# Performance work log

Hardware: AMD Instinct MI355X
Metric: run time of the kernel (lower is better)

The kernel has to match this reference:

```python
import jax, jax.numpy as jnp
import numpy as np
import math

NUM_BUCKETS = 32
MAX_DISTANCE = 128
N_HEADS = 16
D_KV = 64
ATTN_SCALE = True


def _relative_position_bucket(relative_position, num_buckets=NUM_BUCKETS, max_distance=MAX_DISTANCE):
    # bidirectional (encoder) variant
    nb = num_buckets // 2
    buckets = (relative_position > 0).astype(jnp.int32) * nb
    rp = jnp.abs(relative_position)
    max_exact = nb // 2
    is_small = rp < max_exact
    rp_large = max_exact + (
        jnp.log(rp.astype(jnp.float32) / max_exact)
        / math.log(max_distance / max_exact)
        * (nb - max_exact)
    ).astype(jnp.int32)
    rp_large = jnp.minimum(rp_large, nb - 1)
    buckets = buckets + jnp.where(is_small, rp, rp_large)
    return buckets


def compute_bias(rel_bias_emb, q_len, k_len):
    ctx = jnp.arange(q_len)[:, None]
    mem = jnp.arange(k_len)[None, :]
    bucket = _relative_position_bucket(mem - ctx)  # [q,k] int32 in [0,32)
    values = rel_bias_emb[bucket]                  # [q,k,H]
    return jnp.transpose(values, (2, 0, 1))[None]  # [1,H,q,k]


def setup_inputs() -> dict:
    key = jax.random.key(0)
    k1, k2, k3, k4 = jax.random.split(key, 4)
    B, S, D = 2, 2048, 1024
    return {
        "hidden_states": jax.random.normal(k1, (B, S, D), jnp.float32),
        "attention_mask": jnp.ones((B, 1, S, S), jnp.float32),
        "W_qkv": jax.random.normal(k2, (D, 3 * D), jnp.float32) * 0.02,
        "W_o": jax.random.normal(k3, (D, D), jnp.float32) * 0.02,
        "rel_bias_emb": jax.random.normal(k4, (NUM_BUCKETS, N_HEADS), jnp.float32) * 0.02,
    }


def reference(hidden_states, attention_mask, W_qkv, W_o, rel_bias_emb):
    B, S, D = hidden_states.shape
    # fused QKV projection (no bias), then split as in split_tensor_along_last_dim
    qkv = jnp.einsum("bsd,de->bse", hidden_states, W_qkv)
    q, k, v = jnp.split(qkv, 3, axis=-1)
    # [b,s,H*d] -> [b,H,s,d]
    def to_heads(t):
        return jnp.transpose(t.reshape(B, S, N_HEADS, D_KV), (0, 2, 1, 3))
    q, k, v = to_heads(q), to_heads(k), to_heads(v)
    scores = jnp.einsum("bhqd,bhkd->bhqk", q, k)
    if ATTN_SCALE:
        scores = scores / math.sqrt(D_KV)
    position_bias = compute_bias(rel_bias_emb, S, S)  # [1,H,S,S]
    scores = scores * attention_mask + (-10000.0 * (1.0 - attention_mask) + position_bias)
    probs = jax.nn.softmax(scores, axis=-1)  # dropout = eval mode (identity)
    ctx = jnp.einsum("bhqk,bhkd->bhqd", probs, v)
    ctx = jnp.transpose(ctx, (0, 2, 1, 3)).reshape(B, S, N_HEADS * D_KV)
    attn_output = jnp.einsum("bse,ed->bsd", ctx, W_o)
    return attn_output
```

## Files before the change

kernel.cpp:

```cpp
#include <hip/hip_runtime.h>
#include <cstdint>

#define DEV static __device__ __forceinline__

typedef __bf16 bf16x8 __attribute__((ext_vector_type(8)));
typedef __bf16 bf16x4 __attribute__((ext_vector_type(4)));
typedef short  s16x4  __attribute__((ext_vector_type(4)));
typedef float  f32x4  __attribute__((ext_vector_type(4)));

DEV unsigned short f32_bf16(float f) {
  union { float f; unsigned u; } v; v.f = f;
  unsigned r = v.u + 0x7FFFu + ((v.u >> 16) & 1u);
  return (unsigned short)(r >> 16);
}

DEV void gload16(const void* g, void* lds) {
  __builtin_amdgcn_global_load_lds((__attribute__((address_space(1))) void*)g,
                                   (__attribute__((address_space(3))) void*)lds,
                                   16, 0, 0);
}

DEV float bcast_lane(float v, int srclane) {
  union { float f; int i; } u; u.f = v;
  u.i = __builtin_amdgcn_ds_bpermute(srclane << 2, u.i);
  return u.f;
}

DEV f32x4 mfma16_bf16(bf16x4 a, bf16x4 b, f32x4 c) {
  union { bf16x4 h; s16x4 s; } ua, ub; ua.h = a; ub.h = b;
#if __has_builtin(__builtin_amdgcn_mfma_f32_16x16x16bf16_1k)
  return __builtin_amdgcn_mfma_f32_16x16x16bf16_1k(ua.s, ub.s, c, 0, 0, 0);
#else
  f32x4 d;
  asm("v_mfma_f32_16x16x16_bf16 %0, %1, %2, %3" : "=v"(d) : "v"(ua.s), "v"(ub.s), "v"(c));
  return d;
#endif
}

__global__ void cast_and_check(const float* __restrict__ x, unsigned short* __restrict__ y,
                               const float* __restrict__ m, int* __restrict__ flag) {
  int bx = blockIdx.x;
  if (bx < 4096) {
    int i = bx * 256 + threadIdx.x;
    float4 v = ((const float4*)x)[i];
    uint2 o;
    o.x = (unsigned)f32_bf16(v.x) | ((unsigned)f32_bf16(v.y) << 16);
    o.y = (unsigned)f32_bf16(v.z) | ((unsigned)f32_bf16(v.w) << 16);
    ((uint2*)y)[i] = o;
  } else {
    size_t i = ((size_t)(bx - 4096) * 256 + threadIdx.x) * 4;
    float4 v = *(const float4*)(m + i);
    if (v.x != 1.0f || v.y != 1.0f || v.z != 1.0f || v.w != 1.0f) atomicOr(flag, 1);
  }
}

__global__ void transpose_cast2(const float* __restrict__ W1, unsigned short* __restrict__ WT1,
                                const float* __restrict__ W2, unsigned short* __restrict__ WT2) {
  __shared__ float t[64][65];
  int bx = blockIdx.x;
  const float* W; unsigned short* WT; int N, kb, nb;
  if (bx < 768) { W = W1; WT = WT1; N = 3072; kb = bx & 15; nb = bx >> 4; }
  else { bx -= 768; W = W2; WT = WT2; N = 1024; kb = bx & 15; nb = bx >> 4; }
  const int K = 1024;
  int k0 = kb * 64, n0 = nb * 64;
  int tn = threadIdx.x & 63, tk = threadIdx.x >> 6;
#pragma unroll
  for (int i = 0; i < 64; i += 4)
    t[tk + i][tn] = W[(size_t)(k0 + tk + i) * N + n0 + tn];
  __syncthreads();
  int k2 = (threadIdx.x & 31) * 2, n = threadIdx.x >> 5;
#pragma unroll
  for (int i = 0; i < 64; i += 8) {
    int nn = n + i;
    unsigned o = (unsigned)f32_bf16(t[k2][nn]) | ((unsigned)f32_bf16(t[k2 + 1][nn]) << 16);
    *(unsigned*)&WT[(size_t)(n0 + nn) * K + k0 + k2] = o;
  }
}

template <int MODE, int TN>
__global__ void __launch_bounds__(256) gemm_bt(const unsigned short* __restrict__ A,
                                               const unsigned short* __restrict__ BT,
                                               float* __restrict__ Cout,
                                               unsigned short* __restrict__ Qb,
                                               unsigned short* __restrict__ Kb,
                                               unsigned short* __restrict__ VTb,
                                               int M, int N, int K) {
  constexpr int NT = TN / 32;
  __shared__ __align__(16) unsigned short As[128 * 32];
  __shared__ __align__(16) unsigned short Bs[TN * 32];
  const int tid = threadIdx.x, wave = tid >> 6, lane = tid & 63;
  const int l = lane & 15, quad = lane >> 4;
  const int wm = (wave & 1) * 64, wn = (wave >> 1) * (TN >> 1);
  const int bm = blockIdx.x, bn = blockIdx.y;

  const int srowA = wave * 32 + (lane >> 2);
  const int sswzA = ((lane & 3) ^ (srowA & 3)) * 8;
  const int srowB = (TN == 128) ? srowA : (wave * 16 + (lane >> 2));
  const int sswzB = ((lane & 3) ^ (srowB & 3)) * 8;
  const unsigned short* pA = A + (size_t)(bm * 128 + srowA) * K + sswzA;
  const unsigned short* pB = BT + (size_t)(bn * TN + srowB) * K + sswzB;
  unsigned short* ldsA0 = &As[(wave * 32) * 32];
  unsigned short* ldsA1 = &As[(wave * 32 + 16) * 32];
  unsigned short* ldsB0 = &Bs[((TN == 128 ? wave * 32 : wave * 16)) * 32];
  unsigned short* ldsB1 = &Bs[(wave * 32 + 16) * 32];

  f32x4 acc[4][NT];
#pragma unroll
  for (int i = 0; i < 4; i++)
#pragma unroll
    for (int j = 0; j < NT; j++) { f32x4 z = {0.f, 0.f, 0.f, 0.f}; acc[i][j] = z; }

  for (int kt = 0; kt < K; kt += 32) {
    __syncthreads();
    gload16(pA, ldsA0);
    gload16(pA + (size_t)16 * K, ldsA1);
    gload16(pB, ldsB0);
    if (TN == 128) gload16(pB + (size_t)16 * K, ldsB1);
    pA += 32; pB += 32;
    __syncthreads();
    bf16x8 af[4], bv[NT];
#pragma unroll
    for (int mt = 0; mt < 4; mt++) {
      int r = wm + mt * 16 + l;
      af[mt] = *(const bf16x8*)&As[r * 32 + ((quad ^ (r & 3)) * 8)];
    }
#pragma unroll
    for (int nt = 0; nt < NT; nt++) {
      int r = wn + nt * 16 + l;
      bv[nt] = *(const bf16x8*)&Bs[r * 32 + ((quad ^ (r & 3)) * 8)];
    }
#pragma unroll
    for (int mt = 0; mt < 4; mt++)
#pragma unroll
      for (int nt = 0; nt < NT; nt++)
        acc[mt][nt] = __builtin_amdgcn_mfma_f32_16x16x32_bf16(af[mt], bv[nt], acc[mt][nt], 0, 0, 0);
  }

#pragma unroll
  for (int nt = 0; nt < NT; nt++) {
    const int col = bn * TN + wn + nt * 16 + l;
#pragma unroll
    for (int mt = 0; mt < 4; mt++) {
      const int row0 = bm * 128 + wm + mt * 16 + quad * 4;
      if (MODE == 0) {
#pragma unroll
        for (int r = 0; r < 4; r++)
          Cout[(size_t)(row0 + r) * N + col] = acc[mt][nt][r];
      } else {
        const int bb = row0 >> 11, s = row0 & 2047;
        if (col < 2048) {
          unsigned short* dst = (col < 1024) ? Qb : Kb;
          const int c = col & 1023;
          const size_t off = ((size_t)(bb * 16 + (c >> 6)) * 2048 + s) * 64 + (c & 63);
#pragma unroll
          for (int r = 0; r < 4; r++)
            dst[off + (size_t)r * 64] = f32_bf16(acc[mt][nt][r]);
        } else {
          const int c = col - 2048;
          const size_t off = ((size_t)(bb * 16 + (c >> 6)) * 64 + (c & 63)) * 2048 + s;
          bf16x4 pk;
#pragma unroll
          for (int r = 0; r < 4; r++) pk[r] = (__bf16)acc[mt][nt][r];
          *(bf16x4*)&VTb[off] = pk;
        }
      }
    }
  }
}

__global__ void __launch_bounds__(512, 2) attn(const unsigned short* __restrict__ Qb,
                                               const unsigned short* __restrict__ Kb,
                                               const unsigned short* __restrict__ VTb,
                                               const float* __restrict__ mask,
                                               const float* __restrict__ emb,
                                               const int* __restrict__ mflag,
                                               unsigned short* __restrict__ ctx) {
  __shared__ __align__(16) unsigned short KV[2][16384];
  __shared__ float biasLUT[512];
  __shared__ float Lbuf[128];

  const float LOG2E = 1.4426950408889634f;
  const float c1 = 0.125f * LOG2E;
  const float C2 = 10000.0f * LOG2E;
  const int tid = threadIdx.x, wave = tid >> 6, lane = tid & 63;
  const int g = wave >> 2, gw = wave & 3;
  const int l = lane & 15, quad = lane >> 4;
  const int qt = blockIdx.x & 15, bh = blockIdx.x >> 4;
  const int b = bh >> 4, h = bh & 15;
  const int q0 = qt * 128;

  {
    int rel = tid - 256;
    int rp = rel < 0 ? -rel : rel;
    int off = rp < 8 ? rp
                     : 8 + (rp >= 12) + (rp >= 16) + (rp >= 23) + (rp >= 32) +
                           (rp >= 46) + (rp >= 64) + (rp >= 91);
    int bucket = (rel > 0 ? 16 : 0) + off;
    biasLUT[tid] = emb[bucket * 16 + h] * LOG2E;
  }
  const float satL = emb[15 * 16 + h] * LOG2E;
  const float satH = emb[31 * 16 + h] * LOG2E;
  const int masked = *mflag;

  const unsigned short* qbg = Qb  + ((size_t)(b * 16 + h) * 2048 + q0) * 64;
  const unsigned short* kbg = Kb  + (size_t)(b * 16 + h) * 2048 * 64;
  const unsigned short* vtb = VTb + (size_t)(b * 16 + h) * 64 * 2048;
  const float* mbase = mask + (size_t)b * 2048 * 2048;

  const int rw8 = lane >> 3, c8 = lane & 7;
  const int rw16 = lane >> 4, c16 = lane & 15;

  if (wave < 4) {
#pragma unroll
    for (int j = 0; j < 4; j++) {
      int row = wave * 32 + j * 8 + rw8;
      gload16(qbg + (size_t)row * 64 + ((c8 ^ (row & 7)) * 8), &KV[0][(wave * 32 + j * 8) * 64]);
    }
  }
  __syncthreads();
  bf16x8 qf[2][2];
#pragma unroll
  for (int mtq = 0; mtq < 2; mtq++)
#pragma unroll
    for (int ks = 0; ks < 2; ks++) {
      int row = gw * 32 + mtq * 16 + l;
      qf[mtq][ks] = *(const bf16x8*)&KV[0][row * 64 + (((ks * 4 + quad) ^ (row & 7)) * 8)];
    }

  float lr[2] = {0.f, 0.f};
  f32x4 Oa[2][4];
#pragma unroll
  for (int mt = 0; mt < 2; mt++)
#pragma unroll
    for (int dt = 0; dt < 4; dt++) { f32x4 z = {0.f, 0.f, 0.f, 0.f}; Oa[mt][dt] = z; }

  unsigned short* Ks  = &KV[g][0];
  unsigned short* VTs = &KV[g][8192];

  for (int t = 0; t < 8; t++) {
    const int k0 = (g * 8 + t) * 128;
    __syncthreads();
#pragma unroll
    for (int j = 0; j < 4; j++) {
      int row = gw * 32 + j * 8 + rw8;
      gload16(kbg + (size_t)(k0 + row) * 64 + ((c8 ^ (row & 7)) * 8),
              &Ks[(gw * 32 + j * 8) * 64]);
    }
#pragma unroll
    for (int j = 0; j < 4; j++) {
      int drow = gw * 16 + j * 4 + rw16;
      gload16(vtb + (size_t)drow * 2048 + k0 + ((c16 ^ (drow & 7)) * 8),
              &VTs[(gw * 16 + j * 4) * 128]);
    }
    __syncthreads();

    const int d0 = k0 - q0;
    const bool sat = (d0 >= 256) || (d0 <= -256);
    const float bias_u = d0 > 0 ? satH : satL;
    const int ibase = 256 + d0 + quad * 4 - gw * 32 - l;
    bf16x4 pa[2][8];

#pragma unroll
    for (int ntk = 0; ntk < 8; ntk++) {
      int row = ntk * 16 + l;
      bf16x8 kf0 = *(const bf16x8*)&Ks[row * 64 + ((quad ^ (row & 7)) * 8)];
      bf16x8 kf1 = *(const bf16x8*)&Ks[row * 64 + (((4 + quad) ^ (row & 7)) * 8)];
#pragma unroll
      for (int mtq = 0; mtq < 2; mtq++) {
        f32x4 s = {0.f, 0.f, 0.f, 0.f};
        s = __builtin_amdgcn_mfma_f32_16x16x32_bf16(kf0, qf[mtq][0], s, 0, 0, 0);
        s = __builtin_amdgcn_mfma_f32_16x16x32_bf16(kf1, qf[mtq][1], s, 0, 0, 0);

        const int ib = ibase - mtq * 16 + ntk * 16;
        if (!masked) {
          if (sat) {
#pragma unroll
            for (int r = 0; r < 4; r++) s[r] = fmaf(s[r], c1, bias_u);
          } else {
#pragma unroll
            for (int r = 0; r < 4; r++) s[r] = fmaf(s[r], c1, biasLUT[ib + r]);
          }
        } else {
          const int qg = q0 + gw * 32 + mtq * 16 + l;
          const int kg = k0 + ntk * 16 + quad * 4;
          float4 mv4 = *(const float4*)&mbase[(size_t)qg * 2048 + kg];
#pragma unroll
          for (int r = 0; r < 4; r++) {
            float mv = r == 0 ? mv4.x : (r == 1 ? mv4.y : (r == 2 ? mv4.z : mv4.w));
            float bias = sat ? bias_u : biasLUT[ib + r];
            s[r] = fmaf(s[r], mv * c1, fmaf(mv, C2, bias - C2));
          }
        }
        bf16x4 pk;
        float ls = 0.f;
#pragma unroll
        for (int r = 0; r < 4; r++) {
          float p = __builtin_amdgcn_exp2f(s[r]);
          ls += p;
          pk[r] = (__bf16)p;
        }
        lr[mtq] += ls;
        pa[mtq][ntk] = pk;
      }
    }

#pragma unroll
    for (int ntk = 0; ntk < 8; ntk++) {
      bf16x4 vf[4];
#pragma unroll
      for (int dt = 0; dt < 4; dt++) {
        int drow = dt * 16 + l;
        int ch = (ntk * 2 + (quad >> 1)) ^ (l & 7);
        vf[dt] = *(const bf16x4*)&VTs[drow * 128 + ch * 8 + (quad & 1) * 4];
      }
#pragma unroll
      for (int mtq = 0; mtq < 2; mtq++)
#pragma unroll
        for (int dt = 0; dt < 4; dt++)
          Oa[mtq][dt] = mfma16_bf16(pa[mtq][ntk], vf[dt], Oa[mtq][dt]);
    }
  }

#pragma unroll
  for (int mtq = 0; mtq < 2; mtq++) {
    float v = lr[mtq];
    v += __shfl_xor(v, 16);
    v += __shfl_xor(v, 32);
    lr[mtq] = v;
  }

  float* Obuf = (float*)&KV[1][0];
  __syncthreads();
  if (g == 1) {
#pragma unroll
    for (int mt = 0; mt < 2; mt++) {
#pragma unroll
      for (int dt = 0; dt < 4; dt++) {
        const int qc = gw * 8 + mt * 4 + quad;
        *(f32x4*)&Obuf[(dt * 16 + l) * 128 + ((qc ^ (l & 7)) * 4)] = Oa[mt][dt];
      }
      if (quad == 0) Lbuf[gw * 32 + mt * 16 + l] = lr[mt];
    }
  }
  __syncthreads();
  if (g == 0) {
    float inv[2];
#pragma unroll
    for (int mt = 0; mt < 2; mt++)
      inv[mt] = 1.0f / (lr[mt] + Lbuf[gw * 32 + mt * 16 + l]);
#pragma unroll
    for (int mt = 0; mt < 2; mt++)
#pragma unroll
      for (int dt = 0; dt < 4; dt++) {
        const int qc = gw * 8 + mt * 4 + quad;
        f32x4 o = Oa[mt][dt];
        o += *(const f32x4*)&Obuf[(dt * 16 + l) * 128 + ((qc ^ (l & 7)) * 4)];
#pragma unroll
        for (int r = 0; r < 4; r++) {
          float i_bc = bcast_lane(inv[mt], quad * 4 + r);
          const int qg = q0 + gw * 32 + mt * 16 + quad * 4 + r;
          ctx[(size_t)(b * 2048 + qg) * 1024 + h * 64 + dt * 16 + l] =
              f32_bf16(o[r] * i_bc);
        }
      }
  }
}

extern "C" void kernel_launch(void* const* d_in, const int* in_sizes, int n_in,
                              void* d_out, int out_size, void* d_ws, size_t ws_size,
                              hipStream_t stream) {
  const float* hs   = (const float*)d_in[0];
  const float* mask = (const float*)d_in[1];
  const float* wqkv = (const float*)d_in[2];
  const float* wo   = (const float*)d_in[3];
  const float* emb  = (const float*)d_in[4];
  float* out = (float*)d_out;

  char* ws = (char*)d_ws;
  unsigned short* hB  = (unsigned short*)(ws);
  unsigned short* ctx = (unsigned short*)(ws);
  unsigned short* wqT = (unsigned short*)(ws + 8388608);
  unsigned short* woT = (unsigned short*)(ws + 14680064);
  unsigned short* Qb  = (unsigned short*)(ws + 16777216);
  unsigned short* Kb  = (unsigned short*)(ws + 25165824);
  unsigned short* VTb = (unsigned short*)(ws + 33554432);
  int* mflag          = (int*)(ws + 41943040);
  if (ws_size < 41943044) return;

  hipMemsetAsync(mflag, 0, 4, stream);
  cast_and_check<<<12288, 256, 0, stream>>>(hs, hB, mask, mflag);
  transpose_cast2<<<1024, 256, 0, stream>>>(wqkv, wqT, wo, woT);
  gemm_bt<2, 128><<<dim3(32, 24), 256, 0, stream>>>(hB, wqT, nullptr, Qb, Kb, VTb, 4096, 3072, 1024);
  attn<<<512, 512, 0, stream>>>(Qb, Kb, VTb, mask, emb, mflag, ctx);
  gemm_bt<0, 64><<<dim3(32, 16), 256, 0, stream>>>(ctx, woT, out, nullptr, nullptr, nullptr, 4096, 1024, 1024);
}
```

Measured before the change: 234.8 us.

## Restructure attention into 4-wave blocks with 64x64 tiles and prescaled Q

```diff
diff --git a/kernel.cpp b/kernel.cpp
--- a/kernel.cpp
+++ b/kernel.cpp
@@ -7,6 +7,8 @@
 typedef __bf16 bf16x4 __attribute__((ext_vector_type(4)));
 typedef short  s16x4  __attribute__((ext_vector_type(4)));
 typedef float  f32x4  __attribute__((ext_vector_type(4)));
+
+#define C1L 0.18033688f
 
 DEV unsigned short f32_bf16(float f) {
   union { float f; unsigned u; } v; v.f = f;
@@ -150,11 +152,12 @@
         const int bb = row0 >> 11, s = row0 & 2047;
         if (col < 2048) {
           unsigned short* dst = (col < 1024) ? Qb : Kb;
+          const float sc = (col < 1024) ? C1L : 1.0f;
           const int c = col & 1023;
           const size_t off = ((size_t)(bb * 16 + (c >> 6)) * 2048 + s) * 64 + (c & 63);
 #pragma unroll
           for (int r = 0; r < 4; r++)
-            dst[off + (size_t)r * 64] = f32_bf16(acc[mt][nt][r]);
+            dst[off + (size_t)r * 64] = f32_bf16(acc[mt][nt][r] * sc);
         } else {
           const int c = col - 2048;
           const size_t off = ((size_t)(bb * 16 + (c >> 6)) * 64 + (c & 63)) * 2048 + s;
@@ -168,35 +171,36 @@
   }
 }
 
-__global__ void __launch_bounds__(512, 2) attn(const unsigned short* __restrict__ Qb,
+__global__ void __launch_bounds__(256, 2) attn(const unsigned short* __restrict__ Qb,
                                                const unsigned short* __restrict__ Kb,
                                                const unsigned short* __restrict__ VTb,
                                                const float* __restrict__ mask,
                                                const float* __restrict__ emb,
                                                const int* __restrict__ mflag,
                                                unsigned short* __restrict__ ctx) {
-  __shared__ __align__(16) unsigned short KV[2][16384];
+  __shared__ __align__(16) unsigned short KVbuf[16384];
   __shared__ float biasLUT[512];
   __shared__ float Lbuf[128];
+  unsigned short* Ks  = KVbuf;
+  unsigned short* VTs = KVbuf + 8192;
 
   const float LOG2E = 1.4426950408889634f;
-  const float c1 = 0.125f * LOG2E;
   const float C2 = 10000.0f * LOG2E;
   const int tid = threadIdx.x, wave = tid >> 6, lane = tid & 63;
-  const int g = wave >> 2, gw = wave & 3;
+  const int qi = wave >> 1, kj = wave & 1;
   const int l = lane & 15, quad = lane >> 4;
   const int qt = blockIdx.x & 15, bh = blockIdx.x >> 4;
   const int b = bh >> 4, h = bh & 15;
   const int q0 = qt * 128;
 
-  {
-    int rel = tid - 256;
+  for (int i = tid; i < 512; i += 256) {
+    int rel = i - 256;
     int rp = rel < 0 ? -rel : rel;
     int off = rp < 8 ? rp
                      : 8 + (rp >= 12) + (rp >= 16) + (rp >= 23) + (rp >= 32) +
                            (rp >= 46) + (rp >= 64) + (rp >= 91);
     int bucket = (rel > 0 ? 16 : 0) + off;
-    biasLUT[tid] = emb[bucket * 16 + h] * LOG2E;
+    biasLUT[i] = emb[bucket * 16 + h] * LOG2E;
   }
   const float satL = emb[15 * 16 + h] * LOG2E;
   const float satH = emb[31 * 16 + h] * LOG2E;
@@ -210,85 +214,78 @@
   const int rw8 = lane >> 3, c8 = lane & 7;
   const int rw16 = lane >> 4, c16 = lane & 15;
 
-  if (wave < 4) {
+#pragma unroll
+  for (int j = 0; j < 4; j++) {
+    int row = wave * 32 + j * 8 + rw8;
+    gload16(qbg + (size_t)row * 64 + ((c8 ^ (row & 7)) * 8), &Ks[(wave * 32 + j * 8) * 64]);
+  }
+  __syncthreads();
+  bf16x8 qf[4][2];
+#pragma unroll
+  for (int mtq = 0; mtq < 4; mtq++)
+#pragma unroll
+    for (int ks = 0; ks < 2; ks++) {
+      int row = qi * 64 + mtq * 16 + l;
+      qf[mtq][ks] = *(const bf16x8*)&Ks[row * 64 + (((ks * 4 + quad) ^ (row & 7)) * 8)];
+    }
+
+  float lr[4] = {0.f, 0.f, 0.f, 0.f};
+  f32x4 Oa[4][4];
+#pragma unroll
+  for (int mt = 0; mt < 4; mt++)
+#pragma unroll
+    for (int dt = 0; dt < 4; dt++) { f32x4 z = {0.f, 0.f, 0.f, 0.f}; Oa[mt][dt] = z; }
+
+  for (int t = 0; t < 16; t++) {
+    const int k0 = t * 128;
+    __syncthreads();
 #pragma unroll
     for (int j = 0; j < 4; j++) {
       int row = wave * 32 + j * 8 + rw8;
-      gload16(qbg + (size_t)row * 64 + ((c8 ^ (row & 7)) * 8), &KV[0][(wave * 32 + j * 8) * 64]);
-    }
-  }
-  __syncthreads();
-  bf16x8 qf[2][2];
-#pragma unroll
-  for (int mtq = 0; mtq < 2; mtq++)
-#pragma unroll
-    for (int ks = 0; ks < 2; ks++) {
-      int row = gw * 32 + mtq * 16 + l;
-      qf[mtq][ks] = *(const bf16x8*)&KV[0][row * 64 + (((ks * 4 + quad) ^ (row & 7)) * 8)];
-    }
-
-  float lr[2] = {0.f, 0.f};
-  f32x4 Oa[2][4];
-#pragma unroll
-  for (int mt = 0; mt < 2; mt++)
-#pragma unroll
-    for (int dt = 0; dt < 4; dt++) { f32x4 z = {0.f, 0.f, 0.f, 0.f}; Oa[mt][dt] = z; }
-
-  unsigned short* Ks  = &KV[g][0];
-  unsigned short* VTs = &KV[g][8192];
-
-  for (int t = 0; t < 8; t++) {
-    const int k0 = (g * 8 + t) * 128;
+      gload16(kbg + (size_t)(k0 + row) * 64 + ((c8 ^ (row & 7)) * 8),
+              &Ks[(wave * 32 + j * 8) * 64]);
+    }
+#pragma unroll
+    for (int j = 0; j < 4; j++) {
+      int drow = wave * 16 + j * 4 + rw16;
+      gload16(vtb + (size_t)drow * 2048 + k0 + ((c16 ^ (drow & 7)) * 8),
+              &VTs[(wave * 16 + j * 4) * 128]);
+    }
     __syncthreads();
-#pragma unroll
-    for (int j = 0; j < 4; j++) {
-      int row = gw * 32 + j * 8 + rw8;
-      gload16(kbg + (size_t)(k0 + row) * 64 + ((c8 ^ (row & 7)) * 8),
-              &Ks[(gw * 32 + j * 8) * 64]);
-    }
-#pragma unroll
-    for (int j = 0; j < 4; j++) {
-      int drow = gw * 16 + j * 4 + rw16;
-      gload16(vtb + (size_t)drow * 2048 + k0 + ((c16 ^ (drow & 7)) * 8),
-              &VTs[(gw * 16 + j * 4) * 128]);
-    }
-    __syncthreads();
-
-    const int d0 = k0 - q0;
-    const bool sat = (d0 >= 256) || (d0 <= -256);
-    const float bias_u = d0 > 0 ? satH : satL;
-    const int ibase = 256 + d0 + quad * 4 - gw * 32 - l;
-    bf16x4 pa[2][8];
-
-#pragma unroll
-    for (int ntk = 0; ntk < 8; ntk++) {
-      int row = ntk * 16 + l;
+
+    bf16x4 pa[4][4];
+#pragma unroll
+    for (int ntk = 0; ntk < 4; ntk++) {
+      const int row = kj * 64 + ntk * 16 + l;
       bf16x8 kf0 = *(const bf16x8*)&Ks[row * 64 + ((quad ^ (row & 7)) * 8)];
       bf16x8 kf1 = *(const bf16x8*)&Ks[row * 64 + (((4 + quad) ^ (row & 7)) * 8)];
 #pragma unroll
-      for (int mtq = 0; mtq < 2; mtq++) {
-        f32x4 s = {0.f, 0.f, 0.f, 0.f};
+      for (int mtq = 0; mtq < 4; mtq++) {
+        const int base16 = (k0 + kj * 64 + ntk * 16) - (q0 + qi * 64 + mtq * 16);
+        const bool sat = (base16 >= 106) || (base16 <= -106);
+        const float bias_u = base16 > 0 ? satH : satL;
+        const int ib = 256 + base16 + quad * 4 - l;
+        f32x4 s;
+        if (masked) {
+          f32x4 z = {0.f, 0.f, 0.f, 0.f}; s = z;
+        } else if (sat) {
+          s[0] = bias_u; s[1] = bias_u; s[2] = bias_u; s[3] = bias_u;
+        } else {
+#pragma unroll
+          for (int r = 0; r < 4; r++) s[r] = biasLUT[ib + r];
+        }
         s = __builtin_amdgcn_mfma_f32_16x16x32_bf16(kf0, qf[mtq][0], s, 0, 0, 0);
         s = __builtin_amdgcn_mfma_f32_16x16x32_bf16(kf1, qf[mtq][1], s, 0, 0, 0);
 
-        const int ib = ibase - mtq * 16 + ntk * 16;
-        if (!masked) {
-          if (sat) {
-#pragma unroll
-            for (int r = 0; r < 4; r++) s[r] = fmaf(s[r], c1, bias_u);
-          } else {
-#pragma unroll
-            for (int r = 0; r < 4; r++) s[r] = fmaf(s[r], c1, biasLUT[ib + r]);
-          }
-        } else {
-          const int qg = q0 + gw * 32 + mtq * 16 + l;
-          const int kg = k0 + ntk * 16 + quad * 4;
+        if (masked) {
+          const int qg = q0 + qi * 64 + mtq * 16 + l;
+          const int kg = k0 + kj * 64 + ntk * 16 + quad * 4;
           float4 mv4 = *(const float4*)&mbase[(size_t)qg * 2048 + kg];
 #pragma unroll
           for (int r = 0; r < 4; r++) {
             float mv = r == 0 ? mv4.x : (r == 1 ? mv4.y : (r == 2 ? mv4.z : mv4.w));
             float bias = sat ? bias_u : biasLUT[ib + r];
-            s[r] = fmaf(s[r], mv * c1, fmaf(mv, C2, bias - C2));
+            s[r] = fmaf(s[r], mv, fmaf(mv, C2, bias - C2));
           }
         }
         bf16x4 pk;
@@ -305,16 +302,16 @@
     }
 
 #pragma unroll
-    for (int ntk = 0; ntk < 8; ntk++) {
+    for (int ntk = 0; ntk < 4; ntk++) {
       bf16x4 vf[4];
 #pragma unroll
       for (int dt = 0; dt < 4; dt++) {
         int drow = dt * 16 + l;
-        int ch = (ntk * 2 + (quad >> 1)) ^ (l & 7);
-        vf[dt] = *(const bf16x4*)&VTs[drow * 128 + ch * 8 + (quad & 1) * 4];
+        int ck = kj * 8 + ntk * 2 + (quad >> 1);
+        vf[dt] = *(const bf16x4*)&VTs[drow * 128 + ((ck ^ (l & 7)) * 8) + (quad & 1) * 4];
       }
 #pragma unroll
-      for (int mtq = 0; mtq < 2; mtq++)
+      for (int mtq = 0; mtq < 4; mtq++)
 #pragma unroll
         for (int dt = 0; dt < 4; dt++)
           Oa[mtq][dt] = mfma16_bf16(pa[mtq][ntk], vf[dt], Oa[mtq][dt]);
@@ -322,45 +319,45 @@
   }
 
 #pragma unroll
-  for (int mtq = 0; mtq < 2; mtq++) {
+  for (int mtq = 0; mtq < 4; mtq++) {
     float v = lr[mtq];
     v += __shfl_xor(v, 16);
     v += __shfl_xor(v, 32);
     lr[mtq] = v;
   }
 
-  float* Obuf = (float*)&KV[1][0];
+  float* Obuf = (float*)KVbuf;
   __syncthreads();
-  if (g == 1) {
-#pragma unroll
-    for (int mt = 0; mt < 2; mt++) {
+  if (kj == 1) {
+#pragma unroll
+    for (int mtq = 0; mtq < 4; mtq++) {
+#pragma unroll
+      for (int dt = 0; dt < 4; dt++)
+#pragma unroll
+        for (int r = 0; r < 4; r++) {
+          const int q = qi * 64 + mtq * 16 + quad * 4 + r;
+          Obuf[q * 64 + dt * 16 + l] = Oa[mtq][dt][r];
+        }
+      if (quad == 0) Lbuf[qi * 64 + mtq * 16 + l] = lr[mtq];
+    }
+  }
+  __syncthreads();
+  if (kj == 0) {
+    float inv[4];
+#pragma unroll
+    for (int mtq = 0; mtq < 4; mtq++)
+      inv[mtq] = 1.0f / (lr[mtq] + Lbuf[qi * 64 + mtq * 16 + l]);
+#pragma unroll
+    for (int mtq = 0; mtq < 4; mtq++)
 #pragma unroll
       for (int dt = 0; dt < 4; dt++) {
-        const int qc = gw * 8 + mt * 4 + quad;
-        *(f32x4*)&Obuf[(dt * 16 + l) * 128 + ((qc ^ (l & 7)) * 4)] = Oa[mt][dt];
-      }
-      if (quad == 0) Lbuf[gw * 32 + mt * 16 + l] = lr[mt];
-    }
-  }
-  __syncthreads();
-  if (g == 0) {
-    float inv[2];
-#pragma unroll
-    for (int mt = 0; mt < 2; mt++)
-      inv[mt] = 1.0f / (lr[mt] + Lbuf[gw * 32 + mt * 16 + l]);
-#pragma unroll
-    for (int mt = 0; mt < 2; mt++)
-#pragma unroll
-      for (int dt = 0; dt < 4; dt++) {
-        const int qc = gw * 8 + mt * 4 + quad;
-        f32x4 o = Oa[mt][dt];
-        o += *(const f32x4*)&Obuf[(dt * 16 + l) * 128 + ((qc ^ (l & 7)) * 4)];
 #pragma unroll
         for (int r = 0; r < 4; r++) {
-          float i_bc = bcast_lane(inv[mt], quad * 4 + r);
-          const int qg = q0 + gw * 32 + mt * 16 + quad * 4 + r;
-          ctx[(size_t)(b * 2048 + qg) * 1024 + h * 64 + dt * 16 + l] =
-              f32_bf16(o[r] * i_bc);
+          const int q = qi * 64 + mtq * 16 + quad * 4 + r;
+          float o = Oa[mtq][dt][r] + Obuf[q * 64 + dt * 16 + l];
+          float i_bc = bcast_lane(inv[mtq], quad * 4 + r);
+          const int qg = q0 + q;
+          ctx[(size_t)(b * 2048 + qg) * 1024 + h * 64 + dt * 16 + l] = f32_bf16(o * i_bc);
         }
       }
   }
@@ -391,6 +388,6 @@
   cast_and_check<<<12288, 256, 0, stream>>>(hs, hB, mask, mflag);
   transpose_cast2<<<1024, 256, 0, stream>>>(wqkv, wqT, wo, woT);
   gemm_bt<2, 128><<<dim3(32, 24), 256, 0, stream>>>(hB, wqT, nullptr, Qb, Kb, VTb, 4096, 3072, 1024);
-  attn<<<512, 512, 0, stream>>>(Qb, Kb, VTb, mask, emb, mflag, ctx);
+  attn<<<512, 256, 0, stream>>>(Qb, Kb, VTb, mask, emb, mflag, ctx);
   gemm_bt<0, 64><<<dim3(32, 16), 256, 0, stream>>>(ctx, woT, out, nullptr, nullptr, nullptr, 4096, 1024, 1024);
 }
```

Measured after the change: 226.8 us. 1.04x faster.
